# Kernel tuning notes

Measured on AMD Instinct MI355X. Metric: run time of the kernel, lower is better.

The kernel has to match this reference:

```python
import jax, jax.numpy as jnp
import numpy as np

N_NUM, N_CAT, CAT_W, N_ICD = 64, 32, 8, 128
BATCH = 131072


def setup_inputs() -> dict:
    key = jax.random.key(0)
    k1, k2, k3, k4, k5 = jax.random.split(key, 5)
    numerical_x = jax.random.normal(k1, (N_NUM, BATCH), dtype=jnp.float32)
    categorical_x = jax.random.uniform(k2, (N_CAT, BATCH, CAT_W), dtype=jnp.float32)
    icd_x = jax.random.normal(k3, (N_ICD, BATCH), dtype=jnp.float32)
    n_feature = N_NUM + N_CAT * CAT_W + N_ICD  # 448
    n_phenotype = N_NUM + N_CAT + N_ICD        # 224
    W = jax.random.normal(k4, (2, n_feature), dtype=jnp.float32)
    M = jax.random.normal(k5, (2, n_phenotype), dtype=jnp.float32)
    return {"numerical_x": numerical_x, "categorical_x": categorical_x,
            "icd_x": icd_x, "W": W, "M": M}


def reference(numerical_x, categorical_x, icd_x, W, M):
    # numerical_x: [n_num, B]; categorical_x: [n_cat, B, w]; icd_x: [n_icd, B]
    n_num = numerical_x.shape[0]
    n_cat, _, w = categorical_x.shape
    # W column layout matches the original sequential consumption order:
    W_num = W[:, :n_num]                                        # [2, n_num]
    W_cat = W[:, n_num:n_num + n_cat * w].reshape(2, n_cat, w)   # [2, n_cat, w]
    W_icd = W[:, n_num + n_cat * w:]                             # [2, n_icd]
    M_num = M[:, :n_num]
    M_cat = M[:, n_num:n_num + n_cat]
    M_icd = M[:, n_num + n_cat:]
    # per-feature: out_j = M[:, j, None] * tanh(W_block @ x_j.T); f = sum_j out_j
    f_num = jnp.einsum('cn,cnb->cb', M_num,
                       jnp.tanh(W_num[:, :, None] * numerical_x[None, :, :]))
    f_cat = jnp.einsum('cg,cgb->cb', M_cat,
                       jnp.tanh(jnp.einsum('cgw,gbw->cgb', W_cat, categorical_x)))
    f_icd = jnp.einsum('cn,cnb->cb', M_icd,
                       jnp.tanh(W_icd[:, :, None] * icd_x[None, :, :]))
    f = f_num + f_cat + f_icd                                    # [2, B]
    # prob = exp(f) / sum_over_classes(exp(f))  == softmax over axis 0
    return jax.nn.softmax(f, axis=0)
```

## Files before the change

kernel.cpp:

```cpp
#include <hip/hip_runtime.h>

#define N_NUM 64
#define N_CAT 32
#define CAT_W 8
#define N_ICD 128
#define BATCH 131072

#define WROW 448
#define MROW 224

__device__ __forceinline__ float fast_tanh(float x) {
    float e = __expf(2.0f * x);
    return 1.0f - 2.0f * __builtin_amdgcn_rcpf(e + 1.0f);
}

__global__ void __launch_bounds__(256)
phenotype_softmax_kernel(const float* __restrict__ num_x,
                         const float* __restrict__ cat_x,
                         const float* __restrict__ icd_x,
                         const float* __restrict__ W,
                         const float* __restrict__ M,
                         float* __restrict__ out) {
    __shared__ float4 sNum[N_NUM];
    __shared__ float4 sIcd[N_ICD];
    __shared__ float4 sCatW[N_CAT][4];
    __shared__ float2 sCatM[N_CAT];

    const int t = threadIdx.x;

    if (t < N_NUM) {
        sNum[t] = make_float4(W[t], W[WROW + t], M[t], M[MROW + t]);
    }
    if (t < N_ICD) {
        sIcd[t] = make_float4(W[320 + t], W[WROW + 320 + t],
                              M[96 + t],  M[MROW + 96 + t]);
    }
    if (t < N_CAT * 4) {
        int g = t >> 2, q = t & 3, w = 2 * q;
        int base = 64 + g * 8 + w;
        sCatW[g][q] = make_float4(W[base],     W[WROW + base],
                                  W[base + 1], W[WROW + base + 1]);
    }
    if (t < N_CAT) {
        sCatM[t] = make_float2(M[64 + t], M[MROW + 64 + t]);
    }
    __syncthreads();

    const int b = blockIdx.x * 256 + t;
    if (b >= BATCH) return;

    float f0 = 0.0f, f1 = 0.0f;

#pragma unroll 16
    for (int n = 0; n < N_NUM; ++n) {
        float x = num_x[n * BATCH + b];
        float4 c = sNum[n];
        f0 = fmaf(c.z, fast_tanh(c.x * x), f0);
        f1 = fmaf(c.w, fast_tanh(c.y * x), f1);
    }

#pragma unroll 4
    for (int g = 0; g < N_CAT; ++g) {
        const float4* vp = reinterpret_cast<const float4*>(cat_x + ((size_t)g * BATCH + b) * CAT_W);
        float4 v0 = vp[0];
        float4 v1 = vp[1];
        float4 p0 = sCatW[g][0];
        float4 p1 = sCatW[g][1];
        float4 p2 = sCatW[g][2];
        float4 p3 = sCatW[g][3];
        float s0, s1;
        s0 = v0.x * p0.x;            s1 = v0.x * p0.y;
        s0 = fmaf(v0.y, p0.z, s0);   s1 = fmaf(v0.y, p0.w, s1);
        s0 = fmaf(v0.z, p1.x, s0);   s1 = fmaf(v0.z, p1.y, s1);
        s0 = fmaf(v0.w, p1.z, s0);   s1 = fmaf(v0.w, p1.w, s1);
        s0 = fmaf(v1.x, p2.x, s0);   s1 = fmaf(v1.x, p2.y, s1);
        s0 = fmaf(v1.y, p2.z, s0);   s1 = fmaf(v1.y, p2.w, s1);
        s0 = fmaf(v1.z, p3.x, s0);   s1 = fmaf(v1.z, p3.y, s1);
        s0 = fmaf(v1.w, p3.z, s0);   s1 = fmaf(v1.w, p3.w, s1);
        float2 m = sCatM[g];
        f0 = fmaf(m.x, fast_tanh(s0), f0);
        f1 = fmaf(m.y, fast_tanh(s1), f1);
    }

#pragma unroll 16
    for (int n = 0; n < N_ICD; ++n) {
        float x = icd_x[n * BATCH + b];
        float4 c = sIcd[n];
        f0 = fmaf(c.z, fast_tanh(c.x * x), f0);
        f1 = fmaf(c.w, fast_tanh(c.y * x), f1);
    }

    float d = f0 - f1;
    float e0 = __expf(-d);
    float e1 = __expf(d);
    out[b]         = __builtin_amdgcn_rcpf(1.0f + e0);
    out[BATCH + b] = __builtin_amdgcn_rcpf(1.0f + e1);
}

extern "C" void kernel_launch(void* const* d_in, const int* in_sizes, int n_in,
                              void* d_out, int out_size, void* d_ws, size_t ws_size,
                              hipStream_t stream) {
    const float* num_x = (const float*)d_in[0];
    const float* cat_x = (const float*)d_in[1];
    const float* icd_x = (const float*)d_in[2];
    const float* W     = (const float*)d_in[3];
    const float* M     = (const float*)d_in[4];
    float* out = (float*)d_out;

    dim3 block(256);
    dim3 grid((BATCH + 255) / 256);
    phenotype_softmax_kernel<<<grid, block, 0, stream>>>(num_x, cat_x, icd_x, W, M, out);
}
```

Before: 45.96 us.

## Split feature reduction across four waves per batch column and combine via LDS

Each block now handles 64 batch columns, and each of its four waves processes a quarter of the numerical, categorical and ICD features. Partial sums are combined through shared memory before the softmax. This fully unrolls the per-wave loops and quadruples the grid, exposing more independent loads per thread and more blocks. The cost is an extra barrier, LDS traffic, and a shared-parameter setup repeated across four times as many blocks. A min-blocks launch bound of 8 is added.

```diff
diff --git a/kernel.cpp b/kernel.cpp
--- a/kernel.cpp
+++ b/kernel.cpp
@@ -14,7 +14,7 @@
     return 1.0f - 2.0f * __builtin_amdgcn_rcpf(e + 1.0f);
 }
 
-__global__ void __launch_bounds__(256)
+__global__ void __launch_bounds__(256, 8)
 phenotype_softmax_kernel(const float* __restrict__ num_x,
                          const float* __restrict__ cat_x,
                          const float* __restrict__ icd_x,
@@ -25,6 +25,7 @@
     __shared__ float4 sIcd[N_ICD];
     __shared__ float4 sCatW[N_CAT][4];
     __shared__ float2 sCatM[N_CAT];
+    __shared__ float2 sPart[4][64];
 
     const int t = threadIdx.x;
 
@@ -46,21 +47,26 @@
     }
     __syncthreads();
 
-    const int b = blockIdx.x * 256 + t;
-    if (b >= BATCH) return;
+    const int wave = t >> 6;
+    const int lane = t & 63;
+    const int b    = blockIdx.x * 64 + lane;
 
     float f0 = 0.0f, f1 = 0.0f;
 
-#pragma unroll 16
-    for (int n = 0; n < N_NUM; ++n) {
-        float x = num_x[n * BATCH + b];
+    const int n0 = wave * 16;
+#pragma unroll
+    for (int i = 0; i < 16; ++i) {
+        int n = n0 + i;
+        float x = num_x[(size_t)n * BATCH + b];
         float4 c = sNum[n];
         f0 = fmaf(c.z, fast_tanh(c.x * x), f0);
         f1 = fmaf(c.w, fast_tanh(c.y * x), f1);
     }
 
-#pragma unroll 4
-    for (int g = 0; g < N_CAT; ++g) {
+    const int g0 = wave * 8;
+#pragma unroll
+    for (int i = 0; i < 8; ++i) {
+        int g = g0 + i;
         const float4* vp = reinterpret_cast<const float4*>(cat_x + ((size_t)g * BATCH + b) * CAT_W);
         float4 v0 = vp[0];
         float4 v1 = vp[1];
@@ -82,19 +88,33 @@
         f1 = fmaf(m.y, fast_tanh(s1), f1);
     }
 
-#pragma unroll 16
-    for (int n = 0; n < N_ICD; ++n) {
-        float x = icd_x[n * BATCH + b];
+    const int m0 = wave * 32;
+#pragma unroll
+    for (int i = 0; i < 32; ++i) {
+        int n = m0 + i;
+        float x = icd_x[(size_t)n * BATCH + b];
         float4 c = sIcd[n];
         f0 = fmaf(c.z, fast_tanh(c.x * x), f0);
         f1 = fmaf(c.w, fast_tanh(c.y * x), f1);
     }
 
-    float d = f0 - f1;
-    float e0 = __expf(-d);
-    float e1 = __expf(d);
-    out[b]         = __builtin_amdgcn_rcpf(1.0f + e0);
-    out[BATCH + b] = __builtin_amdgcn_rcpf(1.0f + e1);
+    sPart[wave][lane] = make_float2(f0, f1);
+    __syncthreads();
+
+    if (t < 64) {
+        float2 p0 = sPart[0][t];
+        float2 p1 = sPart[1][t];
+        float2 p2 = sPart[2][t];
+        float2 p3 = sPart[3][t];
+        float a0 = p0.x + p1.x + p2.x + p3.x;
+        float a1 = p0.y + p1.y + p2.y + p3.y;
+        float d  = a0 - a1;
+        float e0 = __expf(-d);
+        float e1 = __expf(d);
+        int bb = blockIdx.x * 64 + t;
+        out[bb]         = __builtin_amdgcn_rcpf(1.0f + e0);
+        out[BATCH + bb] = __builtin_amdgcn_rcpf(1.0f + e1);
+    }
 }
 
 extern "C" void kernel_launch(void* const* d_in, const int* in_sizes, int n_in,
@@ -108,6 +128,6 @@
     float* out = (float*)d_out;
 
     dim3 block(256);
-    dim3 grid((BATCH + 255) / 256);
+    dim3 grid(BATCH / 64);
     phenotype_softmax_kernel<<<grid, block, 0, stream>>>(num_x, cat_x, icd_x, W, M, out);
 }
```

After: 44.64 us, median of 2. -2.9%, faster.
